# Optimization experiments

Measured on AMD Instinct MI355X. Metric: run time of the kernel, lower is better.

Reference implementation:

```python
import jax, jax.numpy as jnp
import numpy as np
import math

# kinematic tree: parent of each of the 23 joints (parents[i] < i -> topological order)
PARENTS = np.array([-1, 0, 1, 1, 3, 4, 5, 4, 7, 4, 9, 1, 11, 12, 13, 12, 15, 12, 17, 0, 19, 0, 21])
NUM_J = 23
HALF, QUART = math.pi / 2.0, math.pi / 4.0
# (joint slot, scale) for the pose params actually written in the torch forward
POSE_SLOTS = [(0, QUART), (3, HALF), (4, HALF), (5, QUART), (7, QUART), (9, QUART),
              (11, HALF), (12, HALF), (13, QUART), (15, QUART), (17, QUART)]


def _rodrigues(r):
    # r: [..., 3] axis-angle -> [..., 3, 3] rotation matrix
    angle = jnp.sqrt(jnp.sum(r * r, axis=-1) + 1e-16)
    axis = r / angle[..., None]
    s, c = jnp.sin(angle), jnp.cos(angle)
    x, y, z = axis[..., 0], axis[..., 1], axis[..., 2]
    zero = jnp.zeros_like(x)
    K = jnp.stack([jnp.stack([zero, -z, y], -1),
                   jnp.stack([z, zero, -x], -1),
                   jnp.stack([-y, x, zero], -1)], -2)
    I = jnp.eye(3, dtype=r.dtype)
    return I + s[..., None, None] * K + (1.0 - c)[..., None, None] * (K @ K)


def _lbs_forward(vertices, joints, weights, displacement, random_dis, pose_params):
    P = displacement.shape[0]
    dt = vertices.dtype
    # per-joint pose: pi/4 or pi/2 * tanh(param) on the used slots, zeros elsewhere
    pose = jnp.zeros((P, NUM_J, 3), dt)
    for (idx, scale), prm in zip(POSE_SLOTS, pose_params):
        pose = pose.at[:, idx].set(scale * jnp.tanh(prm))
    R = _rodrigues(pose)                                          # [P,J,3,3]
    j = joints[0].astype(dt)                                      # [J,3] rest joints
    rel = jnp.concatenate([j[:1], j[1:] - j[PARENTS[1:]]], 0)     # joint offsets from parent
    top = jnp.concatenate([R, jnp.broadcast_to(rel[None, :, :, None], (P, NUM_J, 3, 1))], -1)
    bot = jnp.broadcast_to(jnp.array([0.0, 0.0, 0.0, 1.0], dt), (P, NUM_J, 1, 4))
    T_local = jnp.concatenate([top, bot], -2)                     # [P,J,4,4]
    # forward-kinematics tree walk (fixed 23-joint chain, parents precede children)
    Gs = [T_local[:, 0]]
    for i in range(1, NUM_J):
        Gs.append(Gs[PARENTS[i]] @ T_local[:, i])
    G = jnp.stack(Gs, 1)                                          # [P,J,4,4]
    posed_joints = G[..., :3, 3]                                  # [P,J,3]
    # A = G - [0 | G_rot @ j_rest]  (keep only the 3x4 part actually needed)
    A = G[:, :, :3, :].at[..., 3].add(-jnp.einsum('pjab,jb->pja', G[:, :, :3, :3], j))  # [P,J,3,4]
    W = weights.astype(dt)
    T = jnp.einsum('vj,pjab->pvab', W, A)                         # [P,V,3,4] skinning transforms
    v = vertices[0]                                               # [V,3]
    v_posed = jnp.einsum('pvij,vj->pvi', T[..., :3], v) + T[..., 3]  # [P,V,3]
    shift = random_dis[:, None, :] + 3.0 * jnp.tanh(displacement)   # [P,1,3]
    return v_posed + shift, posed_joints + shift


def setup_inputs():
    P, V, J = 16, 500000, NUM_J
    key = jax.random.key(0)
    ks = jax.random.split(key, 16)
    w = jax.random.uniform(ks[2], (V, J), jnp.float32)
    inp = {
        'vertices': jax.random.normal(ks[0], (1, V, 3), jnp.float32),
        'joints': jax.random.normal(ks[1], (1, J, 3), jnp.float32),
        'weights': w / jnp.sum(w, -1, keepdims=True),  # convex skinning weights
        'displacement': 0.1 * jax.random.normal(ks[3], (P, 1, 3), jnp.float32),
        'random_dis': jax.random.normal(ks[4], (P, 3), jnp.float32),
    }
    names = ['joint_0', 'joint_3', 'joint_4', 'joint_5', 'joint_7', 'joint_9',
             'joint_11', 'joint_12', 'joint_13', 'joint_15', 'joint_17']
    for i, n in enumerate(names):
        inp[n] = jax.random.normal(ks[5 + i], (P, 3), jnp.float32)
    return inp


def reference(vertices, joints, weights, displacement, random_dis, joint_0, joint_3, joint_4, joint_5, joint_7, joint_9, joint_11, joint_12, joint_13, joint_15, joint_17):
    pose_params = (joint_0, joint_3, joint_4, joint_5, joint_7, joint_9,
                   joint_11, joint_12, joint_13, joint_15, joint_17)
    return _lbs_forward(vertices, joints, weights, displacement, random_dis, pose_params)
```

## Files before the change

### kernel.cpp

```cpp
#include <hip/hip_runtime.h>
#include <hip/hip_bf16.h>

typedef __hip_bfloat16 bf16;

#define P_CNT 16
#define J_CNT 23
#define VB    128
#define VPT   8
#define WSTR  132

struct PosePtrs { const void* p[11]; };

__device__ const int   c_par[J_CNT]  = {-1,0,1,1,3,4,5,4,7,4,9,1,11,12,13,12,15,12,17,0,19,0,21};
__device__ const int   c_slot[J_CNT] = {0,-1,-1,1,2,3,-1,4,-1,5,-1,6,7,8,-1,9,-1,10,-1,-1,-1,-1,-1};
__device__ const float c_scale[11]   = {
    0.7853981633974483f, 1.5707963267948966f, 1.5707963267948966f, 0.7853981633974483f,
    0.7853981633974483f, 0.7853981633974483f, 1.5707963267948966f, 1.5707963267948966f,
    0.7853981633974483f, 0.7853981633974483f, 0.7853981633974483f};

template <bool BF>
__device__ __forceinline__ float ld(const void* p, long long i) {
    if (BF) return __bfloat162float(((const bf16*)p)[i]);
    return ((const float*)p)[i];
}
template <bool BF>
__device__ __forceinline__ void st(void* p, long long i, float v) {
    if (BF) ((bf16*)p)[i] = __float2bfloat16(v);
    else    ((float*)p)[i] = v;
}
__device__ __forceinline__ float bflo(unsigned u) { return __uint_as_float(u << 16); }
__device__ __forceinline__ float bfhi(unsigned u) { return __uint_as_float(u & 0xffff0000u); }
__device__ __forceinline__ unsigned packbf(float a, float b) {
    bf16 ha = __float2bfloat16(a), hb = __float2bfloat16(b);
    unsigned short ua, ub;
    __builtin_memcpy(&ua, &ha, 2); __builtin_memcpy(&ub, &hb, 2);
    return ((unsigned)ub << 16) | (unsigned)ua;
}
__device__ __forceinline__ int swz(int r) { return r ^ (((r >> 5) & 1) << 2); }

template <bool BF>
__device__ __forceinline__ void run(const void* __restrict__ verts,
                                    const void* __restrict__ joints,
                                    const void* __restrict__ weights,
                                    const void* __restrict__ disp,
                                    const void* __restrict__ rdis,
                                    const PosePtrs pp,
                                    void* __restrict__ out, int V,
                                    float* __restrict__ sA,
                                    float* __restrict__ sW,
                                    float* __restrict__ sPose,
                                    float* __restrict__ sSh)
{
    const int t = threadIdx.x;
    const int p = t >> 4, c = t & 15;
    const long long vb = (long long)blockIdx.x * VB;
    const long long v0 = vb + (long long)c * VPT;
    const bool valigned = ((V & 7) == 0);
    const bool full = ((v0 + VPT) <= (long long)V) && valigned;

    float px[VPT], py[VPT], pz[VPT];
    if (full) {
        if (!BF) {
            const float4* vp = (const float4*)((const float*)verts + v0 * 3);
            float4 q0 = vp[0], q1 = vp[1], q2 = vp[2], q3 = vp[3], q4 = vp[4], q5 = vp[5];
            px[0] = q0.x; py[0] = q0.y; pz[0] = q0.z;
            px[1] = q0.w; py[1] = q1.x; pz[1] = q1.y;
            px[2] = q1.z; py[2] = q1.w; pz[2] = q2.x;
            px[3] = q2.y; py[3] = q2.z; pz[3] = q2.w;
            px[4] = q3.x; py[4] = q3.y; pz[4] = q3.z;
            px[5] = q3.w; py[5] = q4.x; pz[5] = q4.y;
            px[6] = q4.z; py[6] = q4.w; pz[6] = q5.x;
            px[7] = q5.y; py[7] = q5.z; pz[7] = q5.w;
        } else {
            const uint4* vp = (const uint4*)((const bf16*)verts + v0 * 3);
            uint4 u0 = vp[0], u1 = vp[1], u2 = vp[2];
            px[0] = bflo(u0.x); py[0] = bfhi(u0.x); pz[0] = bflo(u0.y);
            px[1] = bfhi(u0.y); py[1] = bflo(u0.z); pz[1] = bfhi(u0.z);
            px[2] = bflo(u0.w); py[2] = bfhi(u0.w); pz[2] = bflo(u1.x);
            px[3] = bfhi(u1.x); py[3] = bflo(u1.y); pz[3] = bfhi(u1.y);
            px[4] = bflo(u1.z); py[4] = bfhi(u1.z); pz[4] = bflo(u1.w);
            px[5] = bfhi(u1.w); py[5] = bflo(u2.x); pz[5] = bfhi(u2.x);
            px[6] = bflo(u2.y); py[6] = bfhi(u2.y); pz[6] = bflo(u2.z);
            px[7] = bfhi(u2.z); py[7] = bflo(u2.w); pz[7] = bfhi(u2.w);
        }
    } else {
#pragma unroll
        for (int v = 0; v < VPT; ++v) {
            bool ok = (v0 + v) < (long long)V;
            px[v] = ok ? ld<BF>(verts, (v0 + v) * 3 + 0) : 0.f;
            py[v] = ok ? ld<BF>(verts, (v0 + v) * 3 + 1) : 0.f;
            pz[v] = ok ? ld<BF>(verts, (v0 + v) * 3 + 2) : 0.f;
        }
    }

#pragma unroll
    for (int s = 0; s < 11; ++s) {
        if (t < P_CNT * 3) sPose[s * (P_CNT * 3) + t] = ld<BF>(pp.p[s], t);
    }

    {
        const long long baseF  = vb * J_CNT;
        const long long totalF = (long long)V * J_CNT;
        if (baseF + VB * J_CNT <= totalF) {
            if (!BF) {
                const float4* wp = (const float4*)((const float*)weights + baseF);
#pragma unroll 1
                for (int idx = t; idx < (VB * J_CNT) / 4; idx += 256) {
                    float4 w4 = wp[idx];
                    int e = idx * 4;
                    { int r = (e+0)/J_CNT, j = (e+0)-r*J_CNT; sW[j*WSTR + swz(r)] = w4.x; }
                    { int r = (e+1)/J_CNT, j = (e+1)-r*J_CNT; sW[j*WSTR + swz(r)] = w4.y; }
                    { int r = (e+2)/J_CNT, j = (e+2)-r*J_CNT; sW[j*WSTR + swz(r)] = w4.z; }
                    { int r = (e+3)/J_CNT, j = (e+3)-r*J_CNT; sW[j*WSTR + swz(r)] = w4.w; }
                }
            } else {
                const uint4* wp = (const uint4*)((const bf16*)weights + baseF);
#pragma unroll 1
                for (int idx = t; idx < (VB * J_CNT) / 8; idx += 256) {
                    uint4 u = wp[idx];
                    int e = idx * 8;
                    float f0 = bflo(u.x), f1 = bfhi(u.x), f2 = bflo(u.y), f3 = bfhi(u.y);
                    float f4 = bflo(u.z), f5 = bfhi(u.z), f6 = bflo(u.w), f7 = bfhi(u.w);
                    { int r = (e+0)/J_CNT, j = (e+0)-r*J_CNT; sW[j*WSTR + swz(r)] = f0; }
                    { int r = (e+1)/J_CNT, j = (e+1)-r*J_CNT; sW[j*WSTR + swz(r)] = f1; }
                    { int r = (e+2)/J_CNT, j = (e+2)-r*J_CNT; sW[j*WSTR + swz(r)] = f2; }
                    { int r = (e+3)/J_CNT, j = (e+3)-r*J_CNT; sW[j*WSTR + swz(r)] = f3; }
                    { int r = (e+4)/J_CNT, j = (e+4)-r*J_CNT; sW[j*WSTR + swz(r)] = f4; }
                    { int r = (e+5)/J_CNT, j = (e+5)-r*J_CNT; sW[j*WSTR + swz(r)] = f5; }
                    { int r = (e+6)/J_CNT, j = (e+6)-r*J_CNT; sW[j*WSTR + swz(r)] = f6; }
                    { int r = (e+7)/J_CNT, j = (e+7)-r*J_CNT; sW[j*WSTR + swz(r)] = f7; }
                }
            }
        } else {
#pragma unroll 1
            for (int e = t; e < VB * J_CNT; e += 256) {
                float val = (baseF + e < totalF) ? ld<BF>(weights, baseF + e) : 0.f;
                int r = e / J_CNT, j = e - r * J_CNT;
                sW[j * WSTR + swz(r)] = val;
            }
        }
    }
    __syncthreads();

#pragma unroll 1
    for (int idx = t; idx < P_CNT * J_CNT; idx += 256) {
        int pq = idx / J_CNT, j = idx - pq * J_CNT;
        float rx = 0.f, ry = 0.f, rz = 0.f;
        int s = c_slot[j];
        if (s >= 0) {
            float sc = c_scale[s];
            rx = sc * tanhf(sPose[s * (P_CNT * 3) + pq * 3 + 0]);
            ry = sc * tanhf(sPose[s * (P_CNT * 3) + pq * 3 + 1]);
            rz = sc * tanhf(sPose[s * (P_CNT * 3) + pq * 3 + 2]);
        }
        float ang = sqrtf(rx * rx + ry * ry + rz * rz + 1e-16f);
        float sn = sinf(ang), cs = cosf(ang);
        float C = 1.f - cs, inva = 1.f / ang;
        float x = rx * inva, y = ry * inva, z = rz * inva;
        float t0 = ld<BF>(joints, j * 3 + 0);
        float t1 = ld<BF>(joints, j * 3 + 1);
        float t2 = ld<BF>(joints, j * 3 + 2);
        if (j != 0) {
            int q = c_par[j];
            t0 -= ld<BF>(joints, q * 3 + 0);
            t1 -= ld<BF>(joints, q * 3 + 1);
            t2 -= ld<BF>(joints, q * 3 + 2);
        }
        float* Ar = sA + idx * 12;
        Ar[0]  = 1.f - C * (y * y + z * z); Ar[1]  = -sn * z + C * x * y;       Ar[2]  = sn * y + C * x * z;       Ar[3]  = t0;
        Ar[4]  = sn * z + C * x * y;        Ar[5]  = 1.f - C * (x * x + z * z); Ar[6]  = -sn * x + C * y * z;      Ar[7]  = t1;
        Ar[8]  = -sn * y + C * x * z;       Ar[9]  = sn * x + C * y * z;        Ar[10] = 1.f - C * (x * x + y * y);Ar[11] = t2;
    }
    if (t < P_CNT) {
#pragma unroll
        for (int cc = 0; cc < 3; ++cc)
            sSh[t * 3 + cc] = ld<BF>(rdis, t * 3 + cc) + 3.f * tanhf(ld<BF>(disp, t * 3 + cc));
    }
    __syncthreads();

    if (t < P_CNT) {
        float* Gp = sA + t * (J_CNT * 12);
#pragma unroll 1
        for (int j = 1; j < J_CNT; ++j) {
            const float* Gq = Gp + c_par[j] * 12;
            float* Tj = Gp + j * 12;
            float4 gq0 = *(const float4*)(Gq + 0);
            float4 gq1 = *(const float4*)(Gq + 4);
            float4 gq2 = *(const float4*)(Gq + 8);
            float4 r0 = *(const float4*)(Tj + 0);
            float4 r1 = *(const float4*)(Tj + 4);
            float4 r2 = *(const float4*)(Tj + 8);
            float4 o0, o1, o2;
            o0.x = gq0.x*r0.x + gq0.y*r1.x + gq0.z*r2.x;
            o0.y = gq0.x*r0.y + gq0.y*r1.y + gq0.z*r2.y;
            o0.z = gq0.x*r0.z + gq0.y*r1.z + gq0.z*r2.z;
            o0.w = gq0.x*r0.w + gq0.y*r1.w + gq0.z*r2.w + gq0.w;
            o1.x = gq1.x*r0.x + gq1.y*r1.x + gq1.z*r2.x;
            o1.y = gq1.x*r0.y + gq1.y*r1.y + gq1.z*r2.y;
            o1.z = gq1.x*r0.z + gq1.y*r1.z + gq1.z*r2.z;
            o1.w = gq1.x*r0.w + gq1.y*r1.w + gq1.z*r2.w + gq1.w;
            o2.x = gq2.x*r0.x + gq2.y*r1.x + gq2.z*r2.x;
            o2.y = gq2.x*r0.y + gq2.y*r1.y + gq2.z*r2.y;
            o2.z = gq2.x*r0.z + gq2.y*r1.z + gq2.z*r2.z;
            o2.w = gq2.x*r0.w + gq2.y*r1.w + gq2.z*r2.w + gq2.w;
            *(float4*)(Tj + 0) = o0;
            *(float4*)(Tj + 4) = o1;
            *(float4*)(Tj + 8) = o2;
        }
    }
    __syncthreads();

    {
        const long long pv3 = (long long)P_CNT * V * 3;
#pragma unroll 1
        for (int idx = t; idx < P_CNT * J_CNT; idx += 256) {
            int pq = idx / J_CNT, j = idx - pq * J_CNT;
            float jx = ld<BF>(joints, j * 3 + 0);
            float jy = ld<BF>(joints, j * 3 + 1);
            float jz = ld<BF>(joints, j * 3 + 2);
            float* Ar = sA + idx * 12;
            float g03 = Ar[3], g13 = Ar[7], g23 = Ar[11];
            Ar[3]  = g03 - (Ar[0] * jx + Ar[1] * jy + Ar[2]  * jz);
            Ar[7]  = g13 - (Ar[4] * jx + Ar[5] * jy + Ar[6]  * jz);
            Ar[11] = g23 - (Ar[8] * jx + Ar[9] * jy + Ar[10] * jz);
            if (blockIdx.x == 0) {
                void* out1 = BF ? (void*)((bf16*)out + pv3) : (void*)((float*)out + pv3);
                st<BF>(out1, (long long)idx * 3 + 0, g03 + sSh[pq * 3 + 0]);
                st<BF>(out1, (long long)idx * 3 + 1, g13 + sSh[pq * 3 + 1]);
                st<BF>(out1, (long long)idx * 3 + 2, g23 + sSh[pq * 3 + 2]);
            }
        }
    }
    __syncthreads();

    float ax[VPT], ay[VPT], az[VPT];
#pragma unroll
    for (int v = 0; v < VPT; ++v) { ax[v] = 0.f; ay[v] = 0.f; az[v] = 0.f; }

    const int s4 = ((c >> 2) & 1) << 2;
    const float* WA = sW + (c << 3) + s4;
    const float* WB = sW + (c << 3) + 4 - s4;
    const float* Ap = sA + p * (J_CNT * 12);

#define STEP(vv, wv) { \
        float d0 = fmaf(a0.x, px[vv], fmaf(a0.y, py[vv], fmaf(a0.z, pz[vv], a0.w))); \
        float d1 = fmaf(a1.x, px[vv], fmaf(a1.y, py[vv], fmaf(a1.z, pz[vv], a1.w))); \
        float d2 = fmaf(a2.x, px[vv], fmaf(a2.y, py[vv], fmaf(a2.z, pz[vv], a2.w))); \
        ax[vv] = fmaf(wv, d0, ax[vv]); \
        ay[vv] = fmaf(wv, d1, ay[vv]); \
        az[vv] = fmaf(wv, d2, az[vv]); }

#pragma unroll 2
    for (int j = 0; j < J_CNT; ++j) {
        float4 a0 = *(const float4*)(Ap + j * 12 + 0);
        float4 a1 = *(const float4*)(Ap + j * 12 + 4);
        float4 a2 = *(const float4*)(Ap + j * 12 + 8);
        float4 wA = *(const float4*)(WA + j * WSTR);
        float4 wB = *(const float4*)(WB + j * WSTR);
        STEP(0, wA.x) STEP(1, wA.y) STEP(2, wA.z) STEP(3, wA.w)
        STEP(4, wB.x) STEP(5, wB.y) STEP(6, wB.z) STEP(7, wB.w)
    }
#undef STEP

    const float shx = sSh[p * 3 + 0], shy = sSh[p * 3 + 1], shz = sSh[p * 3 + 2];
#pragma unroll
    for (int v = 0; v < VPT; ++v) { ax[v] += shx; ay[v] += shy; az[v] += shz; }

    const long long obase = ((long long)p * V + v0) * 3;
    if (!BF) {
        if (full) {
            float4* op = (float4*)((float*)out + obase);
            op[0] = make_float4(ax[0], ay[0], az[0], ax[1]);
            op[1] = make_float4(ay[1], az[1], ax[2], ay[2]);
            op[2] = make_float4(az[2], ax[3], ay[3], az[3]);
            op[3] = make_float4(ax[4], ay[4], az[4], ax[5]);
            op[4] = make_float4(ay[5], az[5], ax[6], ay[6]);
            op[5] = make_float4(az[6], ax[7], ay[7], az[7]);
        } else {
#pragma unroll
            for (int v = 0; v < VPT; ++v)
                if (v0 + v < (long long)V) {
                    ((float*)out)[obase + v * 3 + 0] = ax[v];
                    ((float*)out)[obase + v * 3 + 1] = ay[v];
                    ((float*)out)[obase + v * 3 + 2] = az[v];
                }
        }
    } else {
        if (full) {
            uint4* op = (uint4*)((bf16*)out + obase);
            op[0] = make_uint4(packbf(ax[0], ay[0]), packbf(az[0], ax[1]),
                               packbf(ay[1], az[1]), packbf(ax[2], ay[2]));
            op[1] = make_uint4(packbf(az[2], ax[3]), packbf(ay[3], az[3]),
                               packbf(ax[4], ay[4]), packbf(az[4], ax[5]));
            op[2] = make_uint4(packbf(ay[5], az[5]), packbf(ax[6], ay[6]),
                               packbf(az[6], ax[7]), packbf(ay[7], az[7]));
        } else {
#pragma unroll
            for (int v = 0; v < VPT; ++v)
                if (v0 + v < (long long)V) {
                    st<BF>(out, obase + v * 3 + 0, ax[v]);
                    st<BF>(out, obase + v * 3 + 1, ay[v]);
                    st<BF>(out, obase + v * 3 + 2, az[v]);
                }
        }
    }
}

__global__ void __launch_bounds__(256)
__attribute__((amdgpu_waves_per_eu(2, 4)))
lbs_all(
    const void* __restrict__ verts,
    const void* __restrict__ joints,
    const void* __restrict__ weights,
    const void* __restrict__ disp,
    const void* __restrict__ rdis,
    PosePtrs pp,
    void* __restrict__ out,
    int V)
{
    __shared__ __align__(16) float sA[P_CNT * J_CNT * 12];
    __shared__ __align__(16) float sW[J_CNT * WSTR];
    __shared__ float sPose[11 * P_CNT * 3];
    __shared__ float sSh[P_CNT * 3];
    __shared__ int   sFlag;

    if (threadIdx.x == 0) {
        const float* wf = (const float*)weights;
        const bf16*  wb = (const bf16*)weights;
        bool ok_f = true, ok_b = true;
        for (int r = 0; r < 4; ++r) {
            float sf = 0.f, sb = 0.f;
            for (int j = 0; j < J_CNT; ++j) {
                sf += wf[r * J_CNT + j];
                sb += __bfloat162float(wb[r * J_CNT + j]);
            }
            if (!(fabsf(sf - 1.f) < 0.02f)) ok_f = false;
            if (!(fabsf(sb - 1.f) < 0.10f)) ok_b = false;
        }
        sFlag = (!ok_f && ok_b) ? 1 : 0;
    }
    __syncthreads();
    if (sFlag)
        run<true >(verts, joints, weights, disp, rdis, pp, out, V, sA, sW, sPose, sSh);
    else
        run<false>(verts, joints, weights, disp, rdis, pp, out, V, sA, sW, sPose, sSh);
}

extern "C" void kernel_launch(void* const* d_in, const int* in_sizes, int n_in,
                              void* d_out, int out_size, void* d_ws, size_t ws_size,
                              hipStream_t stream) {
    const void* verts   = d_in[0];
    const void* joints  = d_in[1];
    const void* weights = d_in[2];
    const void* disp    = d_in[3];
    const void* rdis    = d_in[4];
    PosePtrs pp;
    for (int i = 0; i < 11; ++i) pp.p[i] = d_in[5 + i];

    int V = in_sizes[0] / 3;
    int G = (V + VB - 1) / VB;
    lbs_all<<<G, 256, 0, stream>>>(verts, joints, weights, disp, rdis, pp, d_out, V);
}
```

Measured before the change: 288.0 us.

## Switch to one-vertex-per-thread skinning that blends transforms before applying them

```diff
diff --git a/kernel.cpp b/kernel.cpp
--- a/kernel.cpp
+++ b/kernel.cpp
@@ -5,9 +5,7 @@
 
 #define P_CNT 16
 #define J_CNT 23
-#define VB    128
-#define VPT   8
-#define WSTR  132
+#define VB    256
 
 struct PosePtrs { const void* p[11]; };
 
@@ -28,15 +26,6 @@
     if (BF) ((bf16*)p)[i] = __float2bfloat16(v);
     else    ((float*)p)[i] = v;
 }
-__device__ __forceinline__ float bflo(unsigned u) { return __uint_as_float(u << 16); }
-__device__ __forceinline__ float bfhi(unsigned u) { return __uint_as_float(u & 0xffff0000u); }
-__device__ __forceinline__ unsigned packbf(float a, float b) {
-    bf16 ha = __float2bfloat16(a), hb = __float2bfloat16(b);
-    unsigned short ua, ub;
-    __builtin_memcpy(&ua, &ha, 2); __builtin_memcpy(&ub, &hb, 2);
-    return ((unsigned)ub << 16) | (unsigned)ua;
-}
-__device__ __forceinline__ int swz(int r) { return r ^ (((r >> 5) & 1) << 2); }
 
 template <bool BF>
 __device__ __forceinline__ void run(const void* __restrict__ verts,
@@ -47,98 +36,20 @@
                                     const PosePtrs pp,
                                     void* __restrict__ out, int V,
                                     float* __restrict__ sA,
-                                    float* __restrict__ sW,
                                     float* __restrict__ sPose,
                                     float* __restrict__ sSh)
 {
     const int t = threadIdx.x;
-    const int p = t >> 4, c = t & 15;
     const long long vb = (long long)blockIdx.x * VB;
-    const long long v0 = vb + (long long)c * VPT;
-    const bool valigned = ((V & 7) == 0);
-    const bool full = ((v0 + VPT) <= (long long)V) && valigned;
-
-    float px[VPT], py[VPT], pz[VPT];
-    if (full) {
-        if (!BF) {
-            const float4* vp = (const float4*)((const float*)verts + v0 * 3);
-            float4 q0 = vp[0], q1 = vp[1], q2 = vp[2], q3 = vp[3], q4 = vp[4], q5 = vp[5];
-            px[0] = q0.x; py[0] = q0.y; pz[0] = q0.z;
-            px[1] = q0.w; py[1] = q1.x; pz[1] = q1.y;
-            px[2] = q1.z; py[2] = q1.w; pz[2] = q2.x;
-            px[3] = q2.y; py[3] = q2.z; pz[3] = q2.w;
-            px[4] = q3.x; py[4] = q3.y; pz[4] = q3.z;
-            px[5] = q3.w; py[5] = q4.x; pz[5] = q4.y;
-            px[6] = q4.z; py[6] = q4.w; pz[6] = q5.x;
-            px[7] = q5.y; py[7] = q5.z; pz[7] = q5.w;
-        } else {
-            const uint4* vp = (const uint4*)((const bf16*)verts + v0 * 3);
-            uint4 u0 = vp[0], u1 = vp[1], u2 = vp[2];
-            px[0] = bflo(u0.x); py[0] = bfhi(u0.x); pz[0] = bflo(u0.y);
-            px[1] = bfhi(u0.y); py[1] = bflo(u0.z); pz[1] = bfhi(u0.z);
-            px[2] = bflo(u0.w); py[2] = bfhi(u0.w); pz[2] = bflo(u1.x);
-            px[3] = bfhi(u1.x); py[3] = bflo(u1.y); pz[3] = bfhi(u1.y);
-            px[4] = bflo(u1.z); py[4] = bfhi(u1.z); pz[4] = bflo(u1.w);
-            px[5] = bfhi(u1.w); py[5] = bflo(u2.x); pz[5] = bfhi(u2.x);
-            px[6] = bflo(u2.y); py[6] = bfhi(u2.y); pz[6] = bflo(u2.z);
-            px[7] = bfhi(u2.z); py[7] = bflo(u2.w); pz[7] = bfhi(u2.w);
-        }
-    } else {
-#pragma unroll
-        for (int v = 0; v < VPT; ++v) {
-            bool ok = (v0 + v) < (long long)V;
-            px[v] = ok ? ld<BF>(verts, (v0 + v) * 3 + 0) : 0.f;
-            py[v] = ok ? ld<BF>(verts, (v0 + v) * 3 + 1) : 0.f;
-            pz[v] = ok ? ld<BF>(verts, (v0 + v) * 3 + 2) : 0.f;
-        }
-    }
 
 #pragma unroll
     for (int s = 0; s < 11; ++s) {
         if (t < P_CNT * 3) sPose[s * (P_CNT * 3) + t] = ld<BF>(pp.p[s], t);
     }
-
-    {
-        const long long baseF  = vb * J_CNT;
-        const long long totalF = (long long)V * J_CNT;
-        if (baseF + VB * J_CNT <= totalF) {
-            if (!BF) {
-                const float4* wp = (const float4*)((const float*)weights + baseF);
-#pragma unroll 1
-                for (int idx = t; idx < (VB * J_CNT) / 4; idx += 256) {
-                    float4 w4 = wp[idx];
-                    int e = idx * 4;
-                    { int r = (e+0)/J_CNT, j = (e+0)-r*J_CNT; sW[j*WSTR + swz(r)] = w4.x; }
-                    { int r = (e+1)/J_CNT, j = (e+1)-r*J_CNT; sW[j*WSTR + swz(r)] = w4.y; }
-                    { int r = (e+2)/J_CNT, j = (e+2)-r*J_CNT; sW[j*WSTR + swz(r)] = w4.z; }
-                    { int r = (e+3)/J_CNT, j = (e+3)-r*J_CNT; sW[j*WSTR + swz(r)] = w4.w; }
-                }
-            } else {
-                const uint4* wp = (const uint4*)((const bf16*)weights + baseF);
-#pragma unroll 1
-                for (int idx = t; idx < (VB * J_CNT) / 8; idx += 256) {
-                    uint4 u = wp[idx];
-                    int e = idx * 8;
-                    float f0 = bflo(u.x), f1 = bfhi(u.x), f2 = bflo(u.y), f3 = bfhi(u.y);
-                    float f4 = bflo(u.z), f5 = bfhi(u.z), f6 = bflo(u.w), f7 = bfhi(u.w);
-                    { int r = (e+0)/J_CNT, j = (e+0)-r*J_CNT; sW[j*WSTR + swz(r)] = f0; }
-                    { int r = (e+1)/J_CNT, j = (e+1)-r*J_CNT; sW[j*WSTR + swz(r)] = f1; }
-                    { int r = (e+2)/J_CNT, j = (e+2)-r*J_CNT; sW[j*WSTR + swz(r)] = f2; }
-                    { int r = (e+3)/J_CNT, j = (e+3)-r*J_CNT; sW[j*WSTR + swz(r)] = f3; }
-                    { int r = (e+4)/J_CNT, j = (e+4)-r*J_CNT; sW[j*WSTR + swz(r)] = f4; }
-                    { int r = (e+5)/J_CNT, j = (e+5)-r*J_CNT; sW[j*WSTR + swz(r)] = f5; }
-                    { int r = (e+6)/J_CNT, j = (e+6)-r*J_CNT; sW[j*WSTR + swz(r)] = f6; }
-                    { int r = (e+7)/J_CNT, j = (e+7)-r*J_CNT; sW[j*WSTR + swz(r)] = f7; }
-                }
-            }
-        } else {
-#pragma unroll 1
-            for (int e = t; e < VB * J_CNT; e += 256) {
-                float val = (baseF + e < totalF) ? ld<BF>(weights, baseF + e) : 0.f;
-                int r = e / J_CNT, j = e - r * J_CNT;
-                sW[j * WSTR + swz(r)] = val;
-            }
-        }
+    if (t < P_CNT) {
+#pragma unroll
+        for (int cc = 0; cc < 3; ++cc)
+            sSh[t * 3 + cc] = ld<BF>(rdis, t * 3 + cc) + 3.f * tanhf(ld<BF>(disp, t * 3 + cc));
     }
     __syncthreads();
 
@@ -167,14 +78,9 @@
             t2 -= ld<BF>(joints, q * 3 + 2);
         }
         float* Ar = sA + idx * 12;
-        Ar[0]  = 1.f - C * (y * y + z * z); Ar[1]  = -sn * z + C * x * y;       Ar[2]  = sn * y + C * x * z;       Ar[3]  = t0;
-        Ar[4]  = sn * z + C * x * y;        Ar[5]  = 1.f - C * (x * x + z * z); Ar[6]  = -sn * x + C * y * z;      Ar[7]  = t1;
-        Ar[8]  = -sn * y + C * x * z;       Ar[9]  = sn * x + C * y * z;        Ar[10] = 1.f - C * (x * x + y * y);Ar[11] = t2;
-    }
-    if (t < P_CNT) {
-#pragma unroll
-        for (int cc = 0; cc < 3; ++cc)
-            sSh[t * 3 + cc] = ld<BF>(rdis, t * 3 + cc) + 3.f * tanhf(ld<BF>(disp, t * 3 + cc));
+        Ar[0]  = 1.f - C * (y * y + z * z); Ar[1]  = -sn * z + C * x * y;       Ar[2]  = sn * y + C * x * z;        Ar[3]  = t0;
+        Ar[4]  = sn * z + C * x * y;        Ar[5]  = 1.f - C * (x * x + z * z); Ar[6]  = -sn * x + C * y * z;       Ar[7]  = t1;
+        Ar[8]  = -sn * y + C * x * z;       Ar[9]  = sn * x + C * y * z;        Ar[10] = 1.f - C * (x * x + y * y); Ar[11] = t2;
     }
     __syncthreads();
 
@@ -233,82 +139,45 @@
     }
     __syncthreads();
 
-    float ax[VPT], ay[VPT], az[VPT];
-#pragma unroll
-    for (int v = 0; v < VPT; ++v) { ax[v] = 0.f; ay[v] = 0.f; az[v] = 0.f; }
-
-    const int s4 = ((c >> 2) & 1) << 2;
-    const float* WA = sW + (c << 3) + s4;
-    const float* WB = sW + (c << 3) + 4 - s4;
-    const float* Ap = sA + p * (J_CNT * 12);
-
-#define STEP(vv, wv) { \
-        float d0 = fmaf(a0.x, px[vv], fmaf(a0.y, py[vv], fmaf(a0.z, pz[vv], a0.w))); \
-        float d1 = fmaf(a1.x, px[vv], fmaf(a1.y, py[vv], fmaf(a1.z, pz[vv], a1.w))); \
-        float d2 = fmaf(a2.x, px[vv], fmaf(a2.y, py[vv], fmaf(a2.z, pz[vv], a2.w))); \
-        ax[vv] = fmaf(wv, d0, ax[vv]); \
-        ay[vv] = fmaf(wv, d1, ay[vv]); \
-        az[vv] = fmaf(wv, d2, az[vv]); }
-
-#pragma unroll 2
-    for (int j = 0; j < J_CNT; ++j) {
-        float4 a0 = *(const float4*)(Ap + j * 12 + 0);
-        float4 a1 = *(const float4*)(Ap + j * 12 + 4);
-        float4 a2 = *(const float4*)(Ap + j * 12 + 8);
-        float4 wA = *(const float4*)(WA + j * WSTR);
-        float4 wB = *(const float4*)(WB + j * WSTR);
-        STEP(0, wA.x) STEP(1, wA.y) STEP(2, wA.z) STEP(3, wA.w)
-        STEP(4, wB.x) STEP(5, wB.y) STEP(6, wB.z) STEP(7, wB.w)
-    }
-#undef STEP
-
-    const float shx = sSh[p * 3 + 0], shy = sSh[p * 3 + 1], shz = sSh[p * 3 + 2];
-#pragma unroll
-    for (int v = 0; v < VPT; ++v) { ax[v] += shx; ay[v] += shy; az[v] += shz; }
-
-    const long long obase = ((long long)p * V + v0) * 3;
-    if (!BF) {
-        if (full) {
-            float4* op = (float4*)((float*)out + obase);
-            op[0] = make_float4(ax[0], ay[0], az[0], ax[1]);
-            op[1] = make_float4(ay[1], az[1], ax[2], ay[2]);
-            op[2] = make_float4(az[2], ax[3], ay[3], az[3]);
-            op[3] = make_float4(ax[4], ay[4], az[4], ax[5]);
-            op[4] = make_float4(ay[5], az[5], ax[6], ay[6]);
-            op[5] = make_float4(az[6], ax[7], ay[7], az[7]);
-        } else {
-#pragma unroll
-            for (int v = 0; v < VPT; ++v)
-                if (v0 + v < (long long)V) {
-                    ((float*)out)[obase + v * 3 + 0] = ax[v];
-                    ((float*)out)[obase + v * 3 + 1] = ay[v];
-                    ((float*)out)[obase + v * 3 + 2] = az[v];
-                }
-        }
-    } else {
-        if (full) {
-            uint4* op = (uint4*)((bf16*)out + obase);
-            op[0] = make_uint4(packbf(ax[0], ay[0]), packbf(az[0], ax[1]),
-                               packbf(ay[1], az[1]), packbf(ax[2], ay[2]));
-            op[1] = make_uint4(packbf(az[2], ax[3]), packbf(ay[3], az[3]),
-                               packbf(ax[4], ay[4]), packbf(az[4], ax[5]));
-            op[2] = make_uint4(packbf(ay[5], az[5]), packbf(ax[6], ay[6]),
-                               packbf(az[6], ax[7]), packbf(ay[7], az[7]));
-        } else {
-#pragma unroll
-            for (int v = 0; v < VPT; ++v)
-                if (v0 + v < (long long)V) {
-                    st<BF>(out, obase + v * 3 + 0, ax[v]);
-                    st<BF>(out, obase + v * 3 + 1, ay[v]);
-                    st<BF>(out, obase + v * 3 + 2, az[v]);
-                }
-        }
-    }
-}
-
-__global__ void __launch_bounds__(256)
-__attribute__((amdgpu_waves_per_eu(2, 4)))
-lbs_all(
+    const long long v = vb + t;
+    if (v >= (long long)V) return;
+
+    float w[J_CNT];
+    const long long wbase = v * J_CNT;
+#pragma unroll
+    for (int j = 0; j < J_CNT; ++j) w[j] = ld<BF>(weights, wbase + j);
+    float x = ld<BF>(verts, v * 3 + 0);
+    float y = ld<BF>(verts, v * 3 + 1);
+    float z = ld<BF>(verts, v * 3 + 2);
+
+    const float4* A4 = (const float4*)sA;
+    for (int p = 0; p < P_CNT; ++p) {
+        const float4* Ap = A4 + p * (J_CNT * 3);
+        float4 t0 = make_float4(0.f, 0.f, 0.f, 0.f);
+        float4 t1 = make_float4(0.f, 0.f, 0.f, 0.f);
+        float4 t2 = make_float4(0.f, 0.f, 0.f, 0.f);
+#pragma unroll
+        for (int j = 0; j < J_CNT; ++j) {
+            float wj = w[j];
+            float4 a0 = Ap[j * 3 + 0], a1 = Ap[j * 3 + 1], a2 = Ap[j * 3 + 2];
+            t0.x = fmaf(wj, a0.x, t0.x); t0.y = fmaf(wj, a0.y, t0.y);
+            t0.z = fmaf(wj, a0.z, t0.z); t0.w = fmaf(wj, a0.w, t0.w);
+            t1.x = fmaf(wj, a1.x, t1.x); t1.y = fmaf(wj, a1.y, t1.y);
+            t1.z = fmaf(wj, a1.z, t1.z); t1.w = fmaf(wj, a1.w, t1.w);
+            t2.x = fmaf(wj, a2.x, t2.x); t2.y = fmaf(wj, a2.y, t2.y);
+            t2.z = fmaf(wj, a2.z, t2.z); t2.w = fmaf(wj, a2.w, t2.w);
+        }
+        float ox = fmaf(t0.x, x, fmaf(t0.y, y, fmaf(t0.z, z, t0.w))) + sSh[p * 3 + 0];
+        float oy = fmaf(t1.x, x, fmaf(t1.y, y, fmaf(t1.z, z, t1.w))) + sSh[p * 3 + 1];
+        float oz = fmaf(t2.x, x, fmaf(t2.y, y, fmaf(t2.z, z, t2.w))) + sSh[p * 3 + 2];
+        long long base = ((long long)p * V + v) * 3;
+        st<BF>(out, base + 0, ox);
+        st<BF>(out, base + 1, oy);
+        st<BF>(out, base + 2, oz);
+    }
+}
+
+__global__ void __launch_bounds__(256) lbs_all(
     const void* __restrict__ verts,
     const void* __restrict__ joints,
     const void* __restrict__ weights,
@@ -319,7 +188,6 @@
     int V)
 {
     __shared__ __align__(16) float sA[P_CNT * J_CNT * 12];
-    __shared__ __align__(16) float sW[J_CNT * WSTR];
     __shared__ float sPose[11 * P_CNT * 3];
     __shared__ float sSh[P_CNT * 3];
     __shared__ int   sFlag;
@@ -341,9 +209,9 @@
     }
     __syncthreads();
     if (sFlag)
-        run<true >(verts, joints, weights, disp, rdis, pp, out, V, sA, sW, sPose, sSh);
+        run<true >(verts, joints, weights, disp, rdis, pp, out, V, sA, sPose, sSh);
     else
-        run<false>(verts, joints, weights, disp, rdis, pp, out, V, sA, sW, sPose, sSh);
+        run<false>(verts, joints, weights, disp, rdis, pp, out, V, sA, sPose, sSh);
 }
 
 extern "C" void kernel_launch(void* const* d_in, const int* in_sizes, int n_in,
```

Result: faster. 269.3 us (-6.5%).
